# Optimization experiments

Hardware: AMD Instinct MI355X
Metric: run time of the kernel (lower is better)

## Reference

```python
import jax, jax.numpy as jnp
import numpy as np

OBS_LEN = 20
PRED_LEN = 30
NUM_MODES = 6
DATA_DIM = 2
DROPOUT_P = 0.25
NEG_SLOPE = 0.01
H_DIM = 256
B = 8192


def setup_inputs() -> dict:
    key = jax.random.key(0)
    ks = jax.random.split(key, 20)
    s = 0.05
    inp = {
        "traj_abs": jax.random.normal(ks[0], (OBS_LEN, B, DATA_DIM), jnp.float32),
        "traj_rel": jax.random.normal(ks[1], (OBS_LEN, B, DATA_DIM), jnp.float32),
        "state_h": jax.random.normal(ks[2], (1, B, H_DIM), jnp.float32),
        "c0": jax.random.normal(ks[3], (NUM_MODES, B, H_DIM), jnp.float32),
        # spatial embedding Linear(40, 40)
        "W_se": jax.random.normal(ks[4], (OBS_LEN * 2, OBS_LEN * 2), jnp.float32) * s,
        "b_se": jax.random.normal(ks[5], (OBS_LEN * 2,), jnp.float32) * s,
        # LSTM weights: input 40 -> hidden 256, gates order i,f,g,o
        "W_ih": jax.random.normal(ks[6], (4 * H_DIM, OBS_LEN * 2), jnp.float32) * s,
        "W_hh": jax.random.normal(ks[7], (4 * H_DIM, H_DIM), jnp.float32) * s,
        "b_ih": jax.random.normal(ks[8], (4 * H_DIM,), jnp.float32) * s,
        "b_hh": jax.random.normal(ks[9], (4 * H_DIM,), jnp.float32) * s,
        # per-mode prediction heads Linear(256, 2)
        "W_pred": jax.random.normal(ks[10], (NUM_MODES, DATA_DIM, H_DIM), jnp.float32) * s,
        "b_pred": jax.random.normal(ks[11], (NUM_MODES, DATA_DIM), jnp.float32) * s,
        # confidence PredictionNet (norm=False), latent = PRED_LEN*DATA_DIM = 60
        "pn_w1": jax.random.normal(ks[12], (PRED_LEN * DATA_DIM, PRED_LEN * DATA_DIM), jnp.float32) * s,
        "pn_b1": jax.random.normal(ks[13], (PRED_LEN * DATA_DIM,), jnp.float32) * s,
        "pn_w2": jax.random.normal(ks[14], (PRED_LEN * DATA_DIM, PRED_LEN * DATA_DIM), jnp.float32) * s,
        "pn_b2": jax.random.normal(ks[15], (PRED_LEN * DATA_DIM,), jnp.float32) * s,
        "pn_wfc": jax.random.normal(ks[16], (1, PRED_LEN * DATA_DIM), jnp.float32) * s,
        "pn_bfc": jax.random.normal(ks[17], (1,), jnp.float32) * s,
    }
    return inp


def _decode(traj_rel, state_h, c0, W_se, b_se, W_ih, W_hh, b_ih, b_hh,
            W_pred, b_pred, pn_w1, pn_b1, pn_w2, pn_b2, pn_wfc, pn_bfc):
    batch = traj_rel.shape[1]
    h0 = state_h[0]  # (B, H)
    keep = 1.0 - DROPOUT_P
    # one dropout key per (mode, step); deterministic stand-in for torch dropout
    keys = jax.random.split(jax.random.key(42), NUM_MODES * PRED_LEN).reshape(NUM_MODES, PRED_LEN)

    def one_mode(Wp, bp, c0m, keys_m):
        def step(carry, key):
            h, c, buf = carry  # buf: (OBS_LEN, B, 2) rolling window of rel displacements
            x = buf.transpose(1, 0, 2).reshape(batch, -1) @ W_se.T + b_se  # (B, 40)
            x = jnp.where(x > 0, x, NEG_SLOPE * x)  # leaky_relu
            mask = jax.random.bernoulli(key, keep, x.shape)
            x = jnp.where(mask, x / keep, 0.0)  # dropout (training=True)
            gates = x @ W_ih.T + b_ih + h @ W_hh.T + b_hh  # (B, 4H)
            i, f, g, o = jnp.split(gates, 4, axis=-1)
            c = jax.nn.sigmoid(f) * c + jax.nn.sigmoid(i) * jnp.tanh(g)
            h = jax.nn.sigmoid(o) * jnp.tanh(c)
            rel = h @ Wp.T + bp  # (B, 2)
            buf = jnp.roll(buf, -1, axis=0).at[-1].set(rel)
            return (h, c, buf), rel

        _, rels = jax.lax.scan(step, (h0, c0m, traj_rel), keys_m)
        return rels  # (PRED_LEN, B, 2)

    rels = jax.vmap(one_mode)(W_pred, b_pred, c0, keys)  # (M, T, B, 2)
    pred = rels.transpose(2, 0, 1, 3)  # (B, M, T, 2)

    # confidence PredictionNet (norm=False)
    x = pred.reshape(batch, NUM_MODES, PRED_LEN * DATA_DIM)
    y = jax.nn.relu(x @ pn_w1.T + pn_b1)
    y = jax.nn.relu(y @ pn_w2.T + pn_b2 + x)
    conf = (y @ pn_wfc.T + pn_bfc).reshape(batch, NUM_MODES)
    conf = jax.nn.softmax(conf, axis=1)
    return pred, conf


def reference(traj_abs, traj_rel, state_h, c0, W_se, b_se, W_ih, W_hh, b_ih, b_hh,
              W_pred, b_pred, pn_w1, pn_b1, pn_w2, pn_b2, pn_wfc, pn_bfc):
    # traj_abs unused in the 'Latent' branch (only its shape is read)
    return _decode(traj_rel, state_h, c0, W_se, b_se, W_ih, W_hh, b_ih, b_hh,
                   W_pred, b_pred, pn_w1, pn_b1, pn_w2, pn_b2, pn_wfc, pn_bfc)
```

## Files before the change

### kernel.cpp

```cpp
#include <hip/hip_runtime.h>
#include <cstdint>

#define JAX_PARTITIONABLE 1

#define OBS_LEN 20
#define PRED_LEN 30
#define NUM_MODES 6
#define BATCH 8192
#define H 256
#define MB (NUM_MODES * BATCH)
#define KPAD 320

typedef __attribute__((ext_vector_type(8))) short bf16x8;
typedef __attribute__((ext_vector_type(4))) float f32x4;

__host__ __device__ inline void tf2x32(uint32_t k0, uint32_t k1, uint32_t c0, uint32_t c1,
                                       uint32_t& o0, uint32_t& o1) {
  uint32_t ks0 = k0, ks1 = k1, ks2 = k0 ^ k1 ^ 0x1BD11BDAu;
  uint32_t x0 = c0 + ks0, x1 = c1 + ks1;
#define TF_R(x, r) (((x) << (r)) | ((x) >> (32 - (r))))
#define TF_RND(r)  { x0 += x1; x1 = TF_R(x1, r); x1 ^= x0; }
  TF_RND(13) TF_RND(15) TF_RND(26) TF_RND(6)   x0 += ks1; x1 += ks2 + 1u;
  TF_RND(17) TF_RND(29) TF_RND(16) TF_RND(24)  x0 += ks2; x1 += ks0 + 2u;
  TF_RND(13) TF_RND(15) TF_RND(26) TF_RND(6)   x0 += ks0; x1 += ks1 + 3u;
  TF_RND(17) TF_RND(29) TF_RND(16) TF_RND(24)  x0 += ks1; x1 += ks2 + 4u;
  TF_RND(13) TF_RND(15) TF_RND(26) TF_RND(6)   x0 += ks2; x1 += ks0 + 5u;
  o0 = x0; o1 = x1;
#undef TF_RND
#undef TF_R
}

__device__ inline void step_key(int m, int t, uint32_t& k0, uint32_t& k1) {
#if JAX_PARTITIONABLE
  tf2x32(0u, 42u, 0u, (uint32_t)(m * PRED_LEN + t), k0, k1);
#else
  int i = m * PRED_LEN + t;
  int n0 = 2 * i, n1 = 2 * i + 1;
  uint32_t a0, a1;
  if (n0 < 180) { tf2x32(0u, 42u, (uint32_t)n0, (uint32_t)(n0 + 180), a0, a1); k0 = a0; }
  else          { tf2x32(0u, 42u, (uint32_t)(n0 - 180), (uint32_t)n0, a0, a1); k0 = a1; }
  if (n1 < 180) { tf2x32(0u, 42u, (uint32_t)n1, (uint32_t)(n1 + 180), a0, a1); k1 = a0; }
  else          { tf2x32(0u, 42u, (uint32_t)(n1 - 180), (uint32_t)n1, a0, a1); k1 = a1; }
#endif
}

__device__ inline uint32_t mask_bits(uint32_t k0, uint32_t k1, uint32_t n) {
#if JAX_PARTITIONABLE
  uint32_t o0, o1;
  tf2x32(k0, k1, 0u, n, o0, o1);
  return o0 ^ o1;
#else
  const uint32_t HALF = (uint32_t)(BATCH * 40 / 2);
  uint32_t o0, o1;
  if (n < HALF) { tf2x32(k0, k1, n, n + HALF, o0, o1); return o0; }
  else          { tf2x32(k0, k1, n - HALF, n, o0, o1); return o1; }
#endif
}

__device__ __forceinline__ float sigf(float x) { return 1.0f / (1.0f + __expf(-x)); }
__device__ __forceinline__ float tanhfast(float x) {
  float e = __expf(-2.0f * fabsf(x));
  float t = (1.0f - e) / (1.0f + e);
  return x >= 0.f ? t : -t;
}
__device__ __forceinline__ ushort f2bf(float f) {
  uint32_t u = __float_as_uint(f);
  uint32_t r = (u + 0x7fffu + ((u >> 16) & 1u)) >> 16;
  return (ushort)r;
}
__device__ __forceinline__ float bf2f(uint32_t u) { return __uint_as_float(u << 16); }

__global__ __launch_bounds__(256) void k_prep(const float* __restrict__ Wih, const float* __restrict__ Whh,
                                              const float* __restrict__ bih, const float* __restrict__ bhh,
                                              ushort* __restrict__ WTb, float* __restrict__ bias) {
  int idx = blockIdx.x * 256 + threadIdx.x;
  if (idx < 1024 * KPAD) {
    int np = idx / KPAD, k = idx - np * KPAD;
    int cg = np >> 7, r = np & 127;
    int nt = r >> 4, col = r & 15;
    int N = (nt & 3) * 256 + cg * 32 + (nt >> 2) * 16 + col;
    float v = (k < 40) ? Wih[N * 40 + k] : (k < 296 ? Whh[N * 256 + (k - 40)] : 0.f);
    WTb[idx] = f2bf(v);
  }
  if (idx < 1024) bias[idx] = bih[idx] + bhh[idx];
}

__global__ __launch_bounds__(256) void k_init(const float* __restrict__ state_h, const float* __restrict__ c0,
                                              float* __restrict__ cst, ushort* __restrict__ Ab0,
                                              ushort* __restrict__ Ab1) {
  int idx = blockIdx.x * 256 + threadIdx.x;
  if (idx < MB * 64) {
    int row = idx >> 6;
    int j4 = (idx & 63) << 2;
    float4 cv = *(const float4*)(c0 + (size_t)idx * 4);
    *(float4*)(cst + (size_t)idx * 4) = cv;
    int b = row & (BATCH - 1);
    float4 hv = *(const float4*)(state_h + (size_t)b * H + j4);
    ushort4 hb = {f2bf(hv.x), f2bf(hv.y), f2bf(hv.z), f2bf(hv.w)};
    *(ushort4*)(Ab0 + (size_t)row * KPAD + 40 + j4) = hb;
  }
  if (idx < MB * 6) {
    int row = idx / 6, p4 = (idx - row * 6) << 2;
    ushort4 z = {0, 0, 0, 0};
    *(ushort4*)(Ab0 + (size_t)row * KPAD + 296 + p4) = z;
    *(ushort4*)(Ab1 + (size_t)row * KPAD + 296 + p4) = z;
  }
}

__global__ __launch_bounds__(256) void k_embed(const float* __restrict__ traj_rel, const float* __restrict__ rels,
                                               const float* __restrict__ Wse, const float* __restrict__ bse,
                                               ushort* __restrict__ Ax, int t) {
  __shared__ float sW[1600];
  __shared__ float sb[40];
  int tid = threadIdx.x;
  for (int i = tid; i < 1600; i += 256) sW[i] = Wse[i];
  if (tid < 40) sb[tid] = bse[tid];
  __syncthreads();
  int gid = blockIdx.x * 256 + tid;
  int b = gid & (BATCH - 1);
  int m = gid >> 13;
  float win[40];
#pragma unroll
  for (int kk = 0; kk < OBS_LEN; kk++) {
    int st = t + kk;
    const float* p = (st < OBS_LEN)
        ? (traj_rel + (((size_t)st * BATCH + b) << 1))
        : (rels + (((size_t)(m * PRED_LEN + (st - OBS_LEN)) * BATCH + b) << 1));
    float2 w = *(const float2*)p;
    win[kk * 2] = w.x; win[kk * 2 + 1] = w.y;
  }
  uint32_t k0, k1;
  step_key(m, t, k0, k1);
  uint32_t nb = (uint32_t)(b * 40);
  ushort* orow = Ax + (size_t)gid * KPAD;
#pragma unroll
  for (int jo = 0; jo < 5; jo++) {
    uint32_t pk[4];
#pragma unroll
    for (int jp = 0; jp < 4; jp++) {
      ushort lo = 0, hi = 0;
#pragma unroll
      for (int ji = 0; ji < 2; ji++) {
        int j = jo * 8 + jp * 2 + ji;
        float a = sb[j];
#pragma unroll
        for (int p = 0; p < 40; p += 4) {
          float4 w = *(const float4*)&sW[j * 40 + p];
          a = fmaf(win[p + 3], w.w, fmaf(win[p + 2], w.z, fmaf(win[p + 1], w.y, fmaf(win[p], w.x, a))));
        }
        a = a > 0.f ? a : 0.01f * a;
        uint32_t bits = mask_bits(k0, k1, nb + (uint32_t)j);
        float u = __uint_as_float((bits >> 9) | 0x3f800000u) - 1.0f;
        ushort r = (u < 0.75f) ? f2bf(a * 1.3333333730697632f) : (ushort)0;
        if (ji == 0) lo = r; else hi = r;
      }
      pk[jp] = (uint32_t)lo | ((uint32_t)hi << 16);
    }
    uint4 v = {pk[0], pk[1], pk[2], pk[3]};
    *(uint4*)(orow + jo * 8) = v;
  }
}

__global__ __launch_bounds__(256, 3) void k_gates(const ushort* __restrict__ Ain, const ushort* __restrict__ WTb,
                                                  const float* __restrict__ bias, float* __restrict__ cst,
                                                  ushort* __restrict__ Anext) {
  __shared__ __align__(16) ushort lA[2][128][32];
  __shared__ __align__(16) ushort lB[2][128][32];
  int tid = threadIdx.x;
  int w = tid >> 6, lane = tid & 63;
  int row0 = blockIdx.x * 128;
  int cg = blockIdx.y;
  int fm = lane & 15, fq = lane >> 4;
  int srow = lane >> 2;
  int sg = (lane & 3) ^ ((lane >> 3) & 3);
  const ushort* gA0 = Ain + (size_t)(row0 + w * 32 + srow) * KPAD + sg * 8;
  const ushort* gA1 = Ain + (size_t)(row0 + w * 32 + 16 + srow) * KPAD + sg * 8;
  const ushort* gB0 = WTb + (size_t)(cg * 128 + w * 32 + srow) * KPAD + sg * 8;
  const ushort* gB1 = WTb + (size_t)(cg * 128 + w * 32 + 16 + srow) * KPAD + sg * 8;

#define STAGE(buf, kt) {                                                                      \
    __builtin_amdgcn_global_load_lds(                                                         \
        (const __attribute__((address_space(1))) uint32_t*)(gA0 + (kt) * 32),                 \
        (__attribute__((address_space(3))) uint32_t*)&lA[buf][w * 32][0], 16, 0, 0);          \
    __builtin_amdgcn_global_load_lds(                                                         \
        (const __attribute__((address_space(1))) uint32_t*)(gA1 + (kt) * 32),                 \
        (__attribute__((address_space(3))) uint32_t*)&lA[buf][w * 32 + 16][0], 16, 0, 0);     \
    __builtin_amdgcn_global_load_lds(                                                         \
        (const __attribute__((address_space(1))) uint32_t*)(gB0 + (kt) * 32),                 \
        (__attribute__((address_space(3))) uint32_t*)&lB[buf][w * 32][0], 16, 0, 0);          \
    __builtin_amdgcn_global_load_lds(                                                         \
        (const __attribute__((address_space(1))) uint32_t*)(gB1 + (kt) * 32),                 \
        (__attribute__((address_space(3))) uint32_t*)&lB[buf][w * 32 + 16][0], 16, 0, 0);     \
  }

  f32x4 zero = {0.f, 0.f, 0.f, 0.f};
  f32x4 acc[2][8];
#pragma unroll
  for (int i = 0; i < 2; i++)
#pragma unroll
    for (int j = 0; j < 8; j++) acc[i][j] = zero;

  STAGE(0, 0);
  STAGE(1, 1);

  int soff = (fq ^ ((fm >> 1) & 3)) * 8;
#pragma unroll
  for (int kt = 0; kt < 10; kt++) {
    int cur = kt & 1;
    if (kt < 9) { asm volatile("s_waitcnt vmcnt(4)" ::: "memory"); }
    else        { asm volatile("s_waitcnt vmcnt(0)" ::: "memory"); }
    __builtin_amdgcn_s_barrier();
    __builtin_amdgcn_sched_barrier(0);
    bf16x8 af[2], bfr[8];
#pragma unroll
    for (int rt = 0; rt < 2; rt++) af[rt] = *(const bf16x8*)&lA[cur][w * 32 + rt * 16 + fm][soff];
#pragma unroll
    for (int nt = 0; nt < 8; nt++) bfr[nt] = *(const bf16x8*)&lB[cur][nt * 16 + fm][soff];
#pragma unroll
    for (int rt = 0; rt < 2; rt++)
#pragma unroll
      for (int nt = 0; nt < 8; nt++)
        acc[rt][nt] = __builtin_amdgcn_mfma_f32_16x16x32_bf16(af[rt], bfr[nt], acc[rt][nt], 0, 0, 0);
    __builtin_amdgcn_sched_barrier(0);
    __builtin_amdgcn_s_barrier();
    if (kt < 8) STAGE(cur, kt + 2);
  }
#undef STAGE

#pragma unroll
  for (int jg = 0; jg < 2; jg++) {
    int jh = cg * 32 + jg * 16 + fm;
    float bi = bias[jh], bfg = bias[256 + jh], bg = bias[512 + jh], bo = bias[768 + jh];
#pragma unroll
    for (int rt = 0; rt < 2; rt++) {
#pragma unroll
      for (int reg = 0; reg < 4; reg++) {
        int row = row0 + w * 32 + rt * 16 + fq * 4 + reg;
        float gi = acc[rt][jg * 4 + 0][reg] + bi;
        float gf = acc[rt][jg * 4 + 1][reg] + bfg;
        float gg = acc[rt][jg * 4 + 2][reg] + bg;
        float go = acc[rt][jg * 4 + 3][reg] + bo;
        size_t ci = (size_t)row * H + jh;
        float cv = cst[ci];
        float c2 = sigf(gf) * cv + sigf(gi) * tanhfast(gg);
        cst[ci] = c2;
        float hn = sigf(go) * tanhfast(c2);
        Anext[(size_t)row * KPAD + 40 + jh] = f2bf(hn);
      }
    }
  }
}

__global__ __launch_bounds__(256) void k_predembed(const ushort* __restrict__ hsrc, const float* __restrict__ Wp,
                                                   const float* __restrict__ bp, float* __restrict__ rels,
                                                   const float* __restrict__ traj_rel,
                                                   const float* __restrict__ Wse, const float* __restrict__ bse,
                                                   ushort* __restrict__ Ax, int t) {
  __shared__ float sW[1600];
  __shared__ float sb[40];
  int tid = threadIdx.x;
  for (int i = tid; i < 1600; i += 256) sW[i] = Wse[i];
  if (tid < 40) sb[tid] = bse[tid];
  __syncthreads();
  int wv = tid >> 6, lane = tid & 63;
  int grp = lane >> 3, lg = lane & 7;
  int row = blockIdx.x * 32 + wv * 8 + grp;
  int m = row / BATCH, b = row & (BATCH - 1);

  const ushort* hr = hsrc + (size_t)row * KPAD + 40 + lg * 32;
  const float* w0 = Wp + m * 512 + lg * 32;
  const float* w1 = w0 + 256;
  float s0 = 0.f, s1 = 0.f;
#pragma unroll
  for (int q = 0; q < 4; q++) {
    uint4 hv = *(const uint4*)(hr + q * 8);
    float h0 = bf2f(hv.x & 0xffffu), h1 = bf2f(hv.x >> 16);
    float h2 = bf2f(hv.y & 0xffffu), h3 = bf2f(hv.y >> 16);
    float h4 = bf2f(hv.z & 0xffffu), h5 = bf2f(hv.z >> 16);
    float h6 = bf2f(hv.w & 0xffffu), h7 = bf2f(hv.w >> 16);
    float4 wa0 = *(const float4*)(w0 + q * 8);
    float4 wa1 = *(const float4*)(w0 + q * 8 + 4);
    float4 wb0 = *(const float4*)(w1 + q * 8);
    float4 wb1 = *(const float4*)(w1 + q * 8 + 4);
    s0 += h0 * wa0.x + h1 * wa0.y + h2 * wa0.z + h3 * wa0.w
        + h4 * wa1.x + h5 * wa1.y + h6 * wa1.z + h7 * wa1.w;
    s1 += h0 * wb0.x + h1 * wb0.y + h2 * wb0.z + h3 * wb0.w
        + h4 * wb1.x + h5 * wb1.y + h6 * wb1.z + h7 * wb1.w;
  }
#pragma unroll
  for (int off = 1; off < 8; off <<= 1) {
    s0 += __shfl_xor(s0, off, 64);
    s1 += __shfl_xor(s1, off, 64);
  }
  float relx = s0 + bp[m * 2];
  float rely = s1 + bp[m * 2 + 1];
  if (lg == 0) {
    *(float2*)(rels + ((size_t)(m * PRED_LEN + t) * BATCH + b) * 2) = make_float2(relx, rely);
  }

  int te = t + 1;
  float win[40];
#pragma unroll
  for (int kk = 0; kk < OBS_LEN; kk++) {
    int st = te + kk;
    float2 w2;
    if (st < OBS_LEN) {
      w2 = *(const float2*)(traj_rel + (((size_t)st * BATCH + b) << 1));
    } else if (st - OBS_LEN == t) {
      w2 = make_float2(relx, rely);
    } else {
      w2 = *(const float2*)(rels + (((size_t)(m * PRED_LEN + (st - OBS_LEN)) * BATCH + b) << 1));
    }
    win[kk * 2] = w2.x; win[kk * 2 + 1] = w2.y;
  }
  uint32_t k0, k1;
  step_key(m, te, k0, k1);
  uint32_t nb = (uint32_t)(b * 40);
  ushort* orow = Ax + (size_t)row * KPAD;
#pragma unroll
  for (int u = 0; u < 5; u++) {
    int j = lg * 5 + u;
    float a = sb[j];
#pragma unroll
    for (int p = 0; p < 40; p += 4) {
      float4 w = *(const float4*)&sW[j * 40 + p];
      a = fmaf(win[p + 3], w.w, fmaf(win[p + 2], w.z, fmaf(win[p + 1], w.y, fmaf(win[p], w.x, a))));
    }
    a = a > 0.f ? a : 0.01f * a;
    uint32_t bits = mask_bits(k0, k1, nb + (uint32_t)j);
    float uu = __uint_as_float((bits >> 9) | 0x3f800000u) - 1.0f;
    orow[j] = (uu < 0.75f) ? f2bf(a * 1.3333333730697632f) : (ushort)0;
  }
}

__global__ __launch_bounds__(256) void k_transconf(const float* __restrict__ rels,
                                                   const float* __restrict__ W1, const float* __restrict__ b1,
                                                   const float* __restrict__ W2, const float* __restrict__ b2,
                                                   const float* __restrict__ wfc, const float* __restrict__ bfc,
                                                   float* __restrict__ out) {
  __shared__ float tile[32][361];
  __shared__ float sW1[3600];
  __shared__ float sW2[3600];
  __shared__ float sb1[60], sb2[60], swfc[60];
  __shared__ float sy1[192][61];
  __shared__ float slg[32][6];
  int tid = threadIdx.x;
  for (int i = tid; i < 3600; i += 256) { sW1[i] = W1[i]; sW2[i] = W2[i]; }
  if (tid < 60) { sb1[tid] = b1[tid]; sb2[tid] = b2[tid]; swfc[tid] = wfc[tid]; }
  int b0 = blockIdx.x * 32;
  for (int i = tid; i < 11520; i += 256) {
    int bl = i & 31, c = i >> 5;
    int mm = c / 60, r = c % 60;
    tile[bl][c] = rels[((size_t)((mm * PRED_LEN + (r >> 1)) * BATCH) + (b0 + bl)) * 2 + (r & 1)];
  }
  __syncthreads();
  for (int i = tid; i < 11520; i += 256) {
    int bl = i / 360, c = i % 360;
    out[(size_t)(b0 + bl) * 360 + c] = tile[bl][c];
  }
  if (tid < 192) {
    int bl = tid / 6, mm = tid - bl * 6;
    int xb = mm * 60;
    for (int q = 0; q < 60; q++) {
      float acl = sb1[q];
#pragma unroll
      for (int p = 0; p < 60; p++) acl = fmaf(tile[bl][xb + p], sW1[q * 60 + p], acl);
      sy1[tid][q] = fmaxf(acl, 0.f);
    }
    float logit = bfc[0];
    for (int q = 0; q < 60; q++) {
      float acl = sb2[q] + tile[bl][xb + q];
#pragma unroll
      for (int p = 0; p < 60; p++) acl = fmaf(sy1[tid][p], sW2[q * 60 + p], acl);
      logit = fmaf(fmaxf(acl, 0.f), swfc[q], logit);
    }
    slg[bl][mm] = logit;
  }
  __syncthreads();
  if (tid < 32) {
    float mx = slg[tid][0];
#pragma unroll
    for (int m = 1; m < 6; m++) mx = fmaxf(mx, slg[tid][m]);
    float e[6], s = 0.f;
#pragma unroll
    for (int m = 0; m < 6; m++) { e[m] = __expf(slg[tid][m] - mx); s += e[m]; }
    float inv = 1.0f / s;
    size_t base = (size_t)BATCH * 360 + (size_t)(b0 + tid) * 6;
#pragma unroll
    for (int m = 0; m < 6; m++) out[base + m] = e[m] * inv;
  }
}

extern "C" void kernel_launch(void* const* d_in, const int* in_sizes, int n_in,
                              void* d_out, int out_size, void* d_ws, size_t ws_size,
                              hipStream_t stream) {
  const float* traj_rel = (const float*)d_in[1];
  const float* state_h  = (const float*)d_in[2];
  const float* c0       = (const float*)d_in[3];
  const float* Wse      = (const float*)d_in[4];
  const float* bse      = (const float*)d_in[5];
  const float* Wih      = (const float*)d_in[6];
  const float* Whh      = (const float*)d_in[7];
  const float* bih      = (const float*)d_in[8];
  const float* bhh      = (const float*)d_in[9];
  const float* Wp       = (const float*)d_in[10];
  const float* bp       = (const float*)d_in[11];
  const float* W1       = (const float*)d_in[12];
  const float* b1       = (const float*)d_in[13];
  const float* W2       = (const float*)d_in[14];
  const float* b2       = (const float*)d_in[15];
  const float* wfc      = (const float*)d_in[16];
  const float* bfc      = (const float*)d_in[17];
  float* out = (float*)d_out;

  float* cst  = (float*)d_ws;
  float* rels = cst + (size_t)MB * H;
  float* bias = rels + (size_t)NUM_MODES * PRED_LEN * BATCH * 2;
  ushort* WTb = (ushort*)(bias + 1024);
  ushort* Ab0 = WTb + (size_t)1024 * KPAD;
  ushort* Ab1 = Ab0 + (size_t)MB * KPAD;

  k_prep<<<1280, 256, 0, stream>>>(Wih, Whh, bih, bhh, WTb, bias);
  k_init<<<12288, 256, 0, stream>>>(state_h, c0, cst, Ab0, Ab1);
  k_embed<<<192, 256, 0, stream>>>(traj_rel, rels, Wse, bse, Ab0, 0);
  for (int t = 0; t < PRED_LEN; t++) {
    ushort* Acur  = (t & 1) ? Ab1 : Ab0;
    ushort* Anext = (t & 1) ? Ab0 : Ab1;
    k_gates<<<dim3(384, 8), 256, 0, stream>>>(Acur, WTb, bias, cst, Anext);
    k_predembed<<<1536, 256, 0, stream>>>(Anext, Wp, bp, rels, traj_rel, Wse, bse, Anext, t);
  }
  k_transconf<<<256, 256, 0, stream>>>(rels, W1, b1, W2, b2, wfc, bfc, out);
}
```

Baseline: 3.121 ms.

## Triple-buffer LDS staging in gates GEMM and vectorize epilogue via interleaved weight columns

Grows the LDS ring from two to three stages so global-to-LDS loads run two K-tiles ahead, with the vmcnt waits adjusted to match. The weight columns are also permuted in prep so each lane owns two adjacent hidden units. That lets the LSTM cell epilogue read and write cell state as float2 and store packed bf16 pairs of h. The extra LDS per block may reduce occupancy under the 3-blocks-per-SM launch bound.

```diff
diff --git a/kernel.cpp b/kernel.cpp
--- a/kernel.cpp
+++ b/kernel.cpp
@@ -78,7 +78,7 @@
     int np = idx / KPAD, k = idx - np * KPAD;
     int cg = np >> 7, r = np & 127;
     int nt = r >> 4, col = r & 15;
-    int N = (nt & 3) * 256 + cg * 32 + (nt >> 2) * 16 + col;
+    int N = (nt & 3) * 256 + cg * 32 + col * 2 + (nt >> 2);
     float v = (k < 40) ? Wih[N * 40 + k] : (k < 296 ? Whh[N * 256 + (k - 40)] : 0.f);
     WTb[idx] = f2bf(v);
   }
@@ -164,8 +164,8 @@
 __global__ __launch_bounds__(256, 3) void k_gates(const ushort* __restrict__ Ain, const ushort* __restrict__ WTb,
                                                   const float* __restrict__ bias, float* __restrict__ cst,
                                                   ushort* __restrict__ Anext) {
-  __shared__ __align__(16) ushort lA[2][128][32];
-  __shared__ __align__(16) ushort lB[2][128][32];
+  __shared__ __align__(16) ushort lA[3][128][32];
+  __shared__ __align__(16) ushort lB[3][128][32];
   int tid = threadIdx.x;
   int w = tid >> 6, lane = tid & 63;
   int row0 = blockIdx.x * 128;
@@ -202,13 +202,15 @@
 
   STAGE(0, 0);
   STAGE(1, 1);
+  STAGE(2, 2);
 
   int soff = (fq ^ ((fm >> 1) & 3)) * 8;
 #pragma unroll
   for (int kt = 0; kt < 10; kt++) {
-    int cur = kt & 1;
-    if (kt < 9) { asm volatile("s_waitcnt vmcnt(4)" ::: "memory"); }
-    else        { asm volatile("s_waitcnt vmcnt(0)" ::: "memory"); }
+    int cur = kt % 3;
+    if (kt <= 7)      { asm volatile("s_waitcnt vmcnt(8)" ::: "memory"); }
+    else if (kt == 8) { asm volatile("s_waitcnt vmcnt(4)" ::: "memory"); }
+    else              { asm volatile("s_waitcnt vmcnt(0)" ::: "memory"); }
     __builtin_amdgcn_s_barrier();
     __builtin_amdgcn_sched_barrier(0);
     bf16x8 af[2], bfr[8];
@@ -223,30 +225,35 @@
         acc[rt][nt] = __builtin_amdgcn_mfma_f32_16x16x32_bf16(af[rt], bfr[nt], acc[rt][nt], 0, 0, 0);
     __builtin_amdgcn_sched_barrier(0);
     __builtin_amdgcn_s_barrier();
-    if (kt < 8) STAGE(cur, kt + 2);
+    if (kt <= 6) STAGE(cur, kt + 3);
   }
 #undef STAGE
 
-#pragma unroll
-  for (int jg = 0; jg < 2; jg++) {
-    int jh = cg * 32 + jg * 16 + fm;
-    float bi = bias[jh], bfg = bias[256 + jh], bg = bias[512 + jh], bo = bias[768 + jh];
-#pragma unroll
-    for (int rt = 0; rt < 2; rt++) {
-#pragma unroll
-      for (int reg = 0; reg < 4; reg++) {
-        int row = row0 + w * 32 + rt * 16 + fq * 4 + reg;
-        float gi = acc[rt][jg * 4 + 0][reg] + bi;
-        float gf = acc[rt][jg * 4 + 1][reg] + bfg;
-        float gg = acc[rt][jg * 4 + 2][reg] + bg;
-        float go = acc[rt][jg * 4 + 3][reg] + bo;
-        size_t ci = (size_t)row * H + jh;
-        float cv = cst[ci];
-        float c2 = sigf(gf) * cv + sigf(gi) * tanhfast(gg);
-        cst[ci] = c2;
-        float hn = sigf(go) * tanhfast(c2);
-        Anext[(size_t)row * KPAD + 40 + jh] = f2bf(hn);
-      }
+  int p = cg * 16 + fm;
+  const float2* bias2 = (const float2*)bias;
+  float2 bi = bias2[p], bff = bias2[128 + p], bgg = bias2[256 + p], boo = bias2[384 + p];
+  float2* cst2 = (float2*)cst;
+#pragma unroll
+  for (int rt = 0; rt < 2; rt++) {
+#pragma unroll
+    for (int reg = 0; reg < 4; reg++) {
+      int row = row0 + w * 32 + rt * 16 + fq * 4 + reg;
+      float2 cv = cst2[(size_t)row * 128 + p];
+      float gi0 = acc[rt][0][reg] + bi.x;
+      float gf0 = acc[rt][1][reg] + bff.x;
+      float gg0 = acc[rt][2][reg] + bgg.x;
+      float go0 = acc[rt][3][reg] + boo.x;
+      float gi1 = acc[rt][4][reg] + bi.y;
+      float gf1 = acc[rt][5][reg] + bff.y;
+      float gg1 = acc[rt][6][reg] + bgg.y;
+      float go1 = acc[rt][7][reg] + boo.y;
+      float c20 = sigf(gf0) * cv.x + sigf(gi0) * tanhfast(gg0);
+      float c21 = sigf(gf1) * cv.y + sigf(gi1) * tanhfast(gg1);
+      cst2[(size_t)row * 128 + p] = make_float2(c20, c21);
+      float hn0 = sigf(go0) * tanhfast(c20);
+      float hn1 = sigf(go1) * tanhfast(c21);
+      uint32_t hp = (uint32_t)f2bf(hn0) | ((uint32_t)f2bf(hn1) << 16);
+      *(uint32_t*)(Anext + (size_t)row * KPAD + 40 + 2 * p) = hp;
     }
   }
 }
```

Result: no change. 3.102 ms (-0.6%).
